# Performance work log

Measured on AMD Instinct MI355X. Metric: run time of the kernel, lower is better.

## Reference

```python
import jax, jax.numpy as jnp
import numpy as np

NUM_HEADS = 16
D_MODEL = 1024
D_K = D_MODEL // NUM_HEADS
EPS = 1e-6


def setup_inputs() -> dict:
    key = jax.random.key(0)
    ks = jax.random.split(key, 12)
    B, S, D = 8, 1024, D_MODEL
    scale = 0.02
    return {
        "query": jax.random.normal(ks[0], (B, S, D), dtype=jnp.float32),
        "key": jax.random.normal(ks[1], (B, S, D), dtype=jnp.float32),
        "value": jax.random.normal(ks[2], (B, S, D), dtype=jnp.float32),
        "policy": jax.random.uniform(ks[3], (B, S, 1), dtype=jnp.float32),
        "wq_w": jax.random.normal(ks[4], (D, D), dtype=jnp.float32) * scale,
        "wq_b": jnp.zeros((D,), dtype=jnp.float32),
        "wk_w": jax.random.normal(ks[5], (D, D), dtype=jnp.float32) * scale,
        "wk_b": jnp.zeros((D,), dtype=jnp.float32),
        "wv_w": jax.random.normal(ks[6], (D, D), dtype=jnp.float32) * scale,
        "wv_b": jnp.zeros((D,), dtype=jnp.float32),
        "dense_w": jax.random.normal(ks[7], (D, D), dtype=jnp.float32) * scale,
        "dense_b": jnp.zeros((D,), dtype=jnp.float32),
    }


def _split_heads(x):
    B, S, D = x.shape
    return x.reshape(B, S, NUM_HEADS, D_K).transpose(0, 2, 1, 3)  # [B,H,S,dk]


def reference(query, key, value, policy, wq_w, wq_b, wk_w, wk_b, wv_w, wv_b, dense_w, dense_b):
    B, S, D = query.shape
    # torch Linear: y = x @ W.T + b
    q = _split_heads(query @ wq_w.T + wq_b)
    k = _split_heads(key @ wk_w.T + wk_b)
    v = _split_heads(value @ wv_w.T + wv_b)

    scores = jnp.einsum("bhqd,bhkd->bhqk", q, k) / jnp.sqrt(jnp.float32(D_K))
    # policy branch: exp * policy normalization (no softmax max-subtraction, faithful)
    attn_policy = policy.reshape(B, 1, 1, S)
    sc = jnp.exp(scores) * attn_policy
    p_attn = (sc + EPS / S) / (jnp.sum(sc, axis=-1, keepdims=True) + EPS)

    x = jnp.einsum("bhqk,bhkd->bhqd", p_attn, v)
    x = x.transpose(0, 2, 1, 3).reshape(B, S, D)
    out = x @ dense_w.T + dense_b  # dropout = identity (eval mode)
    return out
```

## Files before the change

kernel.cpp:

```cpp
#include <hip/hip_runtime.h>


#define Sdim 1024
#define Ddim 1024

typedef unsigned short u16;
typedef float f32x4 __attribute__((ext_vector_type(4)));
typedef float f32x16 __attribute__((ext_vector_type(16)));
typedef __bf16 bf16x8 __attribute__((ext_vector_type(8)));
typedef u16 u16x8 __attribute__((ext_vector_type(8)));
typedef __attribute__((address_space(3))) void lds_void;
typedef __attribute__((address_space(1))) void gbl_void;

__device__ __forceinline__ u16 f2bf(float f) {
    unsigned u = __float_as_uint(f);
    u += 0x7fffu + ((u >> 16) & 1u);
    return (u16)(u >> 16);
}
__device__ __forceinline__ void gld16(const void* g, void* l) {
    __builtin_amdgcn_global_load_lds((const gbl_void*)g, (lds_void*)l, 16, 0, 0);
}
__device__ __forceinline__ unsigned pk_bf16(float lo, float hi) {
    const unsigned ul = __float_as_uint(lo) + 0x8000u;
    const unsigned uh = __float_as_uint(hi) + 0x8000u;
    return __builtin_amdgcn_perm(uh, ul, 0x07060302u);
}
#define MFMA16(a, b, c) __builtin_amdgcn_mfma_f32_16x16x32_bf16((a), (b), (c), 0, 0, 0)
#define MFMA32(a, b, c) __builtin_amdgcn_mfma_f32_32x32x16_bf16((a), (b), (c), 0, 0, 0)

__global__ __launch_bounds__(256) void cvt_all(const float* __restrict__ s0,
                                               const float* __restrict__ s1,
                                               const float* __restrict__ s2,
                                               const float* __restrict__ s3,
                                               const float* __restrict__ s4,
                                               const float* __restrict__ s5,
                                               const float* __restrict__ s6,
                                               u16* __restrict__ d0, u16* __restrict__ d1,
                                               u16* __restrict__ d2, u16* __restrict__ d3,
                                               u16* __restrict__ d4, u16* __restrict__ d5,
                                               u16* __restrict__ d6) {
    const int z = blockIdx.y;
    if (z >= 3 && blockIdx.x >= 512) return;
    const float* s = z == 0 ? s0 : z == 1 ? s1 : z == 2 ? s2 : z == 3 ? s3
                   : z == 4 ? s4 : z == 5 ? s5 : s6;
    u16* d = z == 0 ? d0 : z == 1 ? d1 : z == 2 ? d2 : z == 3 ? d3
           : z == 4 ? d4 : z == 5 ? d5 : d6;
    const float sc = (z == 3) ? 0.125f : 1.0f;
    const int i = (blockIdx.x * 256 + threadIdx.x) * 8;
    const float4 a = *(const float4*)(s + i);
    const float4 b = *(const float4*)(s + i + 4);
    u16x8 o;
    o[0] = f2bf(a.x * sc); o[1] = f2bf(a.y * sc); o[2] = f2bf(a.z * sc); o[3] = f2bf(a.w * sc);
    o[4] = f2bf(b.x * sc); o[5] = f2bf(b.y * sc); o[6] = f2bf(b.z * sc); o[7] = f2bf(b.w * sc);
    *(u16x8*)(d + i) = o;
}

template <int MODE>
__device__ __forceinline__ void gemm_core(const u16* __restrict__ A,
                                          const u16* __restrict__ W,
                                          const float* __restrict__ bias, float bscale,
                                          void* __restrict__ Cout,
                                          u16* sbuf, int m0, int n0) {
    u16* As = sbuf;
    u16* Bs = sbuf + 4096;
    const int tid  = threadIdx.x;
    const int wave = tid >> 6;
    const int lane = tid & 63;
    const int l15  = lane & 15;
    const int quad = lane >> 4;
    const int wm = (wave >> 1) * 64;
    const int wn = (wave & 1) * 64;

    const int e0 = wave * 512 + lane * 8;
    const int r0 = e0 >> 5, c0 = e0 & 31;
    const int e1 = 2048 + e0;
    const int r1 = e1 >> 5, c1 = e1 & 31;
    const u16* Ag0 = A + (size_t)(m0 + r0) * Ddim + c0;
    const u16* Ag1 = A + (size_t)(m0 + r1) * Ddim + c1;
    const u16* Wg0 = W + (size_t)(n0 + r0) * Ddim + c0;
    const u16* Wg1 = W + (size_t)(n0 + r1) * Ddim + c1;
    u16* As0 = As + wave * 512;
    u16* As1 = As + 2048 + wave * 512;
    u16* Bs0 = Bs + wave * 512;
    u16* Bs1 = Bs + 2048 + wave * 512;

    f32x4 acc[4][4] = {};

    for (int k0 = 0; k0 < Ddim; k0 += 32) {
        __syncthreads();
        gld16(Ag0 + k0, As0);
        gld16(Ag1 + k0, As1);
        gld16(Wg0 + k0, Bs0);
        gld16(Wg1 + k0, Bs1);
        __syncthreads();
        bf16x8 af[4], bfr[4];
#pragma unroll
        for (int i = 0; i < 4; ++i)
            af[i] = *(const bf16x8*)(As + (wm + i * 16 + l15) * 32 + quad * 8);
#pragma unroll
        for (int j = 0; j < 4; ++j)
            bfr[j] = *(const bf16x8*)(Bs + (wn + j * 16 + l15) * 32 + quad * 8);
#pragma unroll
        for (int i = 0; i < 4; ++i)
#pragma unroll
            for (int j = 0; j < 4; ++j)
                acc[i][j] = MFMA16(af[i], bfr[j], acc[i][j]);
    }

    float bv[4];
#pragma unroll
    for (int j = 0; j < 4; ++j) bv[j] = bias[n0 + wn + j * 16 + l15] * bscale;

    if (MODE == 2) {
        __syncthreads();
        u16* Ts = sbuf;
#pragma unroll
        for (int i = 0; i < 4; ++i)
#pragma unroll
            for (int j = 0; j < 4; ++j)
#pragma unroll
                for (int r = 0; r < 4; ++r)
                    Ts[(wm + i * 16 + quad * 4 + r) * 136 + wn + j * 16 + l15] =
                        f2bf(acc[i][j][r] + bv[j]);
        __syncthreads();
        const int orow = tid >> 1;
        const int p    = orow >> 6;
        const int dkl  = orow & 63;
        const int sh   = (tid & 1) * 64;
        const int bidx = m0 >> 10;
        const int s0   = m0 & 1023;
        const int h    = (n0 >> 6) + p;
        u16* dst = (u16*)Cout + ((size_t)((bidx * 16 + h) * 64 + dkl)) * Sdim + s0 + sh;
#pragma unroll
        for (int g = 0; g < 8; ++g) {
            u16x8 o;
#pragma unroll
            for (int j8 = 0; j8 < 8; ++j8)
                o[j8] = Ts[(sh + g * 8 + j8) * 136 + p * 64 + dkl];
            *(u16x8*)(dst + g * 8) = o;
        }
    } else {
#pragma unroll
        for (int i = 0; i < 4; ++i)
#pragma unroll
            for (int j = 0; j < 4; ++j)
#pragma unroll
                for (int r = 0; r < 4; ++r) {
                    const int row = m0 + wm + i * 16 + quad * 4 + r;
                    const int col = n0 + wn + j * 16 + l15;
                    const float v = acc[i][j][r] + bv[j];
                    if (MODE == 0)
                        ((u16*)Cout)[(size_t)row * Ddim + col] = f2bf(v);
                    else
                        ((float*)Cout)[(size_t)row * Ddim + col] = v;
                }
    }
}

__global__ __launch_bounds__(256) void gemm_qkv(const u16* __restrict__ A0, const u16* __restrict__ A1,
                                                const u16* __restrict__ A2,
                                                const u16* __restrict__ W0, const u16* __restrict__ W1,
                                                const u16* __restrict__ W2,
                                                const float* __restrict__ b0, const float* __restrict__ b1,
                                                const float* __restrict__ b2,
                                                u16* __restrict__ Qp, u16* __restrict__ Kp,
                                                u16* __restrict__ Vt) {
    __shared__ __align__(16) u16 sbuf[17408];
    const int z = blockIdx.z;
    const int m0 = blockIdx.x * 128, n0 = blockIdx.y * 128;
    if (z == 2) {
        gemm_core<2>(A2, W2, b2, 1.0f, (void*)Vt, sbuf, m0, n0);
    } else {
        const u16* A = z ? A1 : A0;
        const u16* W = z ? W1 : W0;
        const float* bias = z ? b1 : b0;
        u16* C = z ? Kp : Qp;
        gemm_core<0>(A, W, bias, z ? 1.0f : 0.125f, (void*)C, sbuf, m0, n0);
    }
}

__global__ __launch_bounds__(256) void gemm_dense(const u16* __restrict__ A,
                                                  const u16* __restrict__ W,
                                                  const float* __restrict__ bias,
                                                  float* __restrict__ C) {
    __shared__ __align__(16) u16 sbuf[8192];
    gemm_core<1>(A, W, bias, 1.0f, (void*)C, sbuf, blockIdx.x * 128, blockIdx.y * 128);
}

__global__ __launch_bounds__(256, 2) void attn_mfma(const u16* __restrict__ Qp,
                                                    const u16* __restrict__ Kp,
                                                    const u16* __restrict__ Vt,
                                                    const float* __restrict__ pol,
                                                    u16* __restrict__ Xb) {
    __shared__ __align__(16) u16 lds[28288];
    u16* Qs = lds;
    u16* Ks = lds + 18432;
    u16* Vs = lds + 23040;
    float* pols = (float*)(lds + 27648);
    float* denb = pols + 64;

    const int tid  = threadIdx.x;
    const int w    = tid >> 6;
    const int lane = tid & 63;
    const int l31  = lane & 31;
    const unsigned hsel = lane >> 5;
    const int q0 = blockIdx.x * 256;
    const int bh = blockIdx.y;
    const size_t bS = (size_t)(bh >> 4) * Sdim;
    const int col0 = (bh & 15) * 64;
    const int sr = tid >> 2;
    const int sc4 = tid & 3;

#pragma unroll
    for (int rg = 0; rg < 4; ++rg) {
        const int r = rg * 64 + sr;
#pragma unroll
        for (int g = 0; g < 2; ++g) {
            const int ch = sc4 + g * 4;
            *(u16x8*)(Qs + r * 72 + ch * 8) =
                *(const u16x8*)(Qp + (bS + q0 + r) * Ddim + col0 + ch * 8);
        }
    }
    __syncthreads();
    bf16x8 Qf[2][4];
#pragma unroll
    for (int qt = 0; qt < 2; ++qt)
#pragma unroll
        for (int dkt = 0; dkt < 4; ++dkt)
            Qf[qt][dkt] = *(const bf16x8*)(Qs + (w * 64 + qt * 32 + l31) * 72 +
                                           dkt * 16 + hsel * 8);

    f32x16 X[2][2] = {};
    float den[2] = {0.f, 0.f};

    for (int kt = 0; kt < 16; ++kt) {
        const int kbase = kt * 64;
        __syncthreads();
#pragma unroll
        for (int g = 0; g < 2; ++g) {
            const int ch = sc4 + g * 4;
            *(u16x8*)(Ks + sr * 72 + ch * 8) =
                *(const u16x8*)(Kp + (bS + kbase + sr) * Ddim + col0 + ch * 8);
            *(u16x8*)(Vs + sr * 72 + ch * 8) =
                *(const u16x8*)(Vt + ((size_t)(bh * 64 + sr)) * Sdim + kbase + ch * 8);
        }
        if (tid < 64) pols[tid] = pol[bS + kbase + tid];
        __syncthreads();

#pragma unroll
        for (int t32 = 0; t32 < 2; ++t32) {
            float polv[16];
#pragma unroll
            for (int e = 0; e < 16; ++e)
                polv[e] = pols[t32 * 32 + (e & 3) + 8 * (e >> 2) + 4 * hsel];
            bf16x8 Kf[4];
#pragma unroll
            for (int dkt = 0; dkt < 4; ++dkt)
                Kf[dkt] = *(const bf16x8*)(Ks + (t32 * 32 + l31) * 72 +
                                           dkt * 16 + hsel * 8);
#pragma unroll
            for (int qt = 0; qt < 2; ++qt) {
                f32x16 S = {};
#pragma unroll
                for (int dkt = 0; dkt < 4; ++dkt)
                    S = MFMA32(Kf[dkt], Qf[qt][dkt], S);
                float p[16];
#pragma unroll
                for (int e = 0; e < 16; ++e) {
                    p[e] = __expf(S[e]) * polv[e];
                    den[qt] += p[e];
                }
                unsigned pk_[8], sw[8];
#pragma unroll
                for (int g = 0; g < 4; ++g) {
                    pk_[2 * g]     = pk_bf16(p[4 * g + 0], p[4 * g + 1]);
                    pk_[2 * g + 1] = pk_bf16(p[4 * g + 2], p[4 * g + 3]);
                }
#pragma unroll
                for (int i = 0; i < 8; ++i)
                    sw[i] = (unsigned)__shfl_xor((int)pk_[i], 32);
#pragma unroll
                for (int tau = 0; tau < 2; ++tau) {
                    union { unsigned u[4]; bf16x8 v; } Af;
                    Af.u[0] = hsel ? sw[(2 * tau + 1) * 2 + 0] : pk_[(2 * tau) * 2 + 0];
                    Af.u[1] = hsel ? sw[(2 * tau + 1) * 2 + 1] : pk_[(2 * tau) * 2 + 1];
                    Af.u[2] = hsel ? pk_[(2 * tau + 1) * 2 + 0] : sw[(2 * tau) * 2 + 0];
                    Af.u[3] = hsel ? pk_[(2 * tau + 1) * 2 + 1] : sw[(2 * tau) * 2 + 1];
#pragma unroll
                    for (int ndt = 0; ndt < 2; ++ndt) {
                        const bf16x8 Vf =
                            *(const bf16x8*)(Vs + (ndt * 32 + l31) * 72 +
                                             t32 * 32 + tau * 16 + hsel * 8);
                        X[qt][ndt] = MFMA32(Af.v, Vf, X[qt][ndt]);
                    }
                }
            }
        }
    }

#pragma unroll
    for (int qt = 0; qt < 2; ++qt) {
        den[qt] += __shfl_xor(den[qt], 32);
        denb[w * 64 + qt * 32 + l31] = 1.0f / (den[qt] + 1e-6f);
    }
    u16* Xout = Qs;
#pragma unroll
    for (int qt = 0; qt < 2; ++qt) {
        float invv[16];
#pragma unroll
        for (int e = 0; e < 16; ++e)
            invv[e] = denb[w * 64 + qt * 32 + (e & 3) + 8 * (e >> 2) + 4 * hsel];
#pragma unroll
        for (int ndt = 0; ndt < 2; ++ndt)
#pragma unroll
            for (int e = 0; e < 16; ++e) {
                const int rho = (e & 3) + 8 * (e >> 2) + 4 * hsel;
                Xout[(w * 64 + qt * 32 + rho) * 72 + ndt * 32 + l31] =
                    f2bf(X[qt][ndt][e] * invv[e]);
            }
    }
    __syncthreads();
#pragma unroll
    for (int rg = 0; rg < 4; ++rg) {
        const int r = rg * 64 + sr;
#pragma unroll
        for (int g = 0; g < 2; ++g) {
            const int ch = sc4 + g * 4;
            *(u16x8*)(Xb + (bS + q0 + r) * Ddim + col0 + ch * 8) =
                *(const u16x8*)(Xout + r * 72 + ch * 8);
        }
    }
}

extern "C" void kernel_launch(void* const* d_in, const int* in_sizes, int n_in,
                              void* d_out, int out_size, void* d_ws, size_t ws_size,
                              hipStream_t stream) {
    const float* query   = (const float*)d_in[0];
    const float* key     = (const float*)d_in[1];
    const float* value   = (const float*)d_in[2];
    const float* policy  = (const float*)d_in[3];
    const float* wq_w    = (const float*)d_in[4];
    const float* wq_b    = (const float*)d_in[5];
    const float* wk_w    = (const float*)d_in[6];
    const float* wk_b    = (const float*)d_in[7];
    const float* wv_w    = (const float*)d_in[8];
    const float* wv_b    = (const float*)d_in[9];
    const float* dense_w = (const float*)d_in[10];
    const float* dense_b = (const float*)d_in[11];

    const size_t MM = 1u << 20;
    const size_t A8 = 8 * MM;
    u16* qa  = (u16*)d_ws;
    u16* ka  = qa + A8;
    u16* va  = ka + A8;
    u16* wqb = va + A8;
    u16* wkb = wqb + MM;
    u16* wvb = wkb + MM;
    u16* wdb = wvb + MM;
    u16* Qp  = wdb + MM;
    u16* Kp  = Qp + A8;
    u16* Vtg = Kp + A8;
    u16* Xb  = qa;

    cvt_all<<<dim3(4096, 7), 256, 0, stream>>>(query, key, value, wq_w, wk_w, wv_w, dense_w,
                                               qa, ka, va, wqb, wkb, wvb, wdb);

    gemm_qkv<<<dim3(64, 8, 3), 256, 0, stream>>>(qa, ka, va, wqb, wkb, wvb,
                                                 wq_b, wk_b, wv_b, Qp, Kp, Vtg);

    attn_mfma<<<dim3(4, 128), 256, 0, stream>>>(Qp, Kp, Vtg, policy, Xb);

    gemm_dense<<<dim3(64, 8), 256, 0, stream>>>(Xb, wdb, dense_b, (float*)d_out);
}
```

Measured before the change: 309.9 us.

## Shrink LDS footprint in QKV GEMM and attention, use exp2 with folded scale

The V-transpose epilogue in the QKV GEMM now stages the tile in two halves, so the shared buffer halves in size. The attention kernel no longer stages Q through LDS; it loads Q fragments straight from global memory and writes the output through a half-size buffer in two passes, cutting LDS from about 56KB to about 20KB to allow more resident blocks. log2(e) is folded into the Q scale so the softmax uses the native exp2. Policy and inverse-denominator reads are vectorized, and V fragments are hoisted out of the qt loop. The cost is extra barriers and uncoalesced direct Q loads.

```diff
diff --git a/kernel.cpp b/kernel.cpp
--- a/kernel.cpp
+++ b/kernel.cpp
@@ -3,6 +3,7 @@
 
 #define Sdim 1024
 #define Ddim 1024
+#define QSCALE 0.18033688f
 
 typedef unsigned short u16;
 typedef float f32x4 __attribute__((ext_vector_type(4)));
@@ -45,7 +46,7 @@
                    : z == 4 ? s4 : z == 5 ? s5 : s6;
     u16* d = z == 0 ? d0 : z == 1 ? d1 : z == 2 ? d2 : z == 3 ? d3
            : z == 4 ? d4 : z == 5 ? d5 : d6;
-    const float sc = (z == 3) ? 0.125f : 1.0f;
+    const float sc = (z == 3) ? QSCALE : 1.0f;
     const int i = (blockIdx.x * 256 + threadIdx.x) * 8;
     const float4 a = *(const float4*)(s + i);
     const float4 b = *(const float4*)(s + i + 4);
@@ -112,32 +113,37 @@
     for (int j = 0; j < 4; ++j) bv[j] = bias[n0 + wn + j * 16 + l15] * bscale;
 
     if (MODE == 2) {
-        __syncthreads();
         u16* Ts = sbuf;
-#pragma unroll
-        for (int i = 0; i < 4; ++i)
-#pragma unroll
-            for (int j = 0; j < 4; ++j)
-#pragma unroll
-                for (int r = 0; r < 4; ++r)
-                    Ts[(wm + i * 16 + quad * 4 + r) * 136 + wn + j * 16 + l15] =
-                        f2bf(acc[i][j][r] + bv[j]);
-        __syncthreads();
         const int orow = tid >> 1;
-        const int p    = orow >> 6;
-        const int dkl  = orow & 63;
-        const int sh   = (tid & 1) * 64;
+        const int sh2  = (tid & 1) * 32;
         const int bidx = m0 >> 10;
         const int s0   = m0 & 1023;
-        const int h    = (n0 >> 6) + p;
-        u16* dst = (u16*)Cout + ((size_t)((bidx * 16 + h) * 64 + dkl)) * Sdim + s0 + sh;
-#pragma unroll
-        for (int g = 0; g < 8; ++g) {
-            u16x8 o;
-#pragma unroll
-            for (int j8 = 0; j8 < 8; ++j8)
-                o[j8] = Ts[(sh + g * 8 + j8) * 136 + p * 64 + dkl];
-            *(u16x8*)(dst + g * 8) = o;
+        const int h    = (n0 >> 6) + (orow >> 6);
+        const int dkl  = orow & 63;
+#pragma unroll
+        for (int p = 0; p < 2; ++p) {
+            __syncthreads();
+            if ((wave >> 1) == p) {
+#pragma unroll
+                for (int i = 0; i < 4; ++i)
+#pragma unroll
+                    for (int j = 0; j < 4; ++j)
+#pragma unroll
+                        for (int r = 0; r < 4; ++r)
+                            Ts[(i * 16 + quad * 4 + r) * 136 + wn + j * 16 + l15] =
+                                f2bf(acc[i][j][r] + bv[j]);
+            }
+            __syncthreads();
+            u16* dst = (u16*)Cout +
+                ((size_t)((bidx * 16 + h) * 64 + dkl)) * Sdim + s0 + p * 64 + sh2;
+#pragma unroll
+            for (int g = 0; g < 4; ++g) {
+                u16x8 o;
+#pragma unroll
+                for (int j8 = 0; j8 < 8; ++j8)
+                    o[j8] = Ts[(sh2 + g * 8 + j8) * 136 + orow];
+                *(u16x8*)(dst + g * 8) = o;
+            }
         }
     } else {
 #pragma unroll
@@ -165,7 +171,7 @@
                                                 const float* __restrict__ b2,
                                                 u16* __restrict__ Qp, u16* __restrict__ Kp,
                                                 u16* __restrict__ Vt) {
-    __shared__ __align__(16) u16 sbuf[17408];
+    __shared__ __align__(16) u16 sbuf[8704];
     const int z = blockIdx.z;
     const int m0 = blockIdx.x * 128, n0 = blockIdx.y * 128;
     if (z == 2) {
@@ -175,7 +181,7 @@
         const u16* W = z ? W1 : W0;
         const float* bias = z ? b1 : b0;
         u16* C = z ? Kp : Qp;
-        gemm_core<0>(A, W, bias, z ? 1.0f : 0.125f, (void*)C, sbuf, m0, n0);
+        gemm_core<0>(A, W, bias, z ? 1.0f : QSCALE, (void*)C, sbuf, m0, n0);
     }
 }
 
@@ -192,18 +198,18 @@
                                                     const u16* __restrict__ Vt,
                                                     const float* __restrict__ pol,
                                                     u16* __restrict__ Xb) {
-    __shared__ __align__(16) u16 lds[28288];
-    u16* Qs = lds;
-    u16* Ks = lds + 18432;
-    u16* Vs = lds + 23040;
-    float* pols = (float*)(lds + 27648);
+    __shared__ __align__(16) u16 lds[9856];
+    u16* Ks = lds;
+    u16* Vs = lds + 4608;
+    u16* outb = lds;
+    float* pols = (float*)(lds + 9216);
     float* denb = pols + 64;
 
     const int tid  = threadIdx.x;
     const int w    = tid >> 6;
     const int lane = tid & 63;
     const int l31  = lane & 31;
-    const unsigned hsel = lane >> 5;
+    const int hsel = lane >> 5;
     const int q0 = blockIdx.x * 256;
     const int bh = blockIdx.y;
     const size_t bS = (size_t)(bh >> 4) * Sdim;
@@ -211,24 +217,13 @@
     const int sr = tid >> 2;
     const int sc4 = tid & 3;
 
-#pragma unroll
-    for (int rg = 0; rg < 4; ++rg) {
-        const int r = rg * 64 + sr;
-#pragma unroll
-        for (int g = 0; g < 2; ++g) {
-            const int ch = sc4 + g * 4;
-            *(u16x8*)(Qs + r * 72 + ch * 8) =
-                *(const u16x8*)(Qp + (bS + q0 + r) * Ddim + col0 + ch * 8);
-        }
-    }
-    __syncthreads();
     bf16x8 Qf[2][4];
 #pragma unroll
     for (int qt = 0; qt < 2; ++qt)
 #pragma unroll
         for (int dkt = 0; dkt < 4; ++dkt)
-            Qf[qt][dkt] = *(const bf16x8*)(Qs + (w * 64 + qt * 32 + l31) * 72 +
-                                           dkt * 16 + hsel * 8);
+            Qf[qt][dkt] = *(const bf16x8*)(Qp + (bS + q0 + w * 64 + qt * 32 + l31) * Ddim +
+                                           col0 + dkt * 16 + hsel * 8);
 
     f32x16 X[2][2] = {};
     float den[2] = {0.f, 0.f};
@@ -249,15 +244,21 @@
 
 #pragma unroll
         for (int t32 = 0; t32 < 2; ++t32) {
-            float polv[16];
-#pragma unroll
-            for (int e = 0; e < 16; ++e)
-                polv[e] = pols[t32 * 32 + (e & 3) + 8 * (e >> 2) + 4 * hsel];
+            f32x4 pv4[4];
+#pragma unroll
+            for (int j = 0; j < 4; ++j)
+                pv4[j] = *(const f32x4*)&pols[t32 * 32 + 8 * j + 4 * hsel];
             bf16x8 Kf[4];
 #pragma unroll
             for (int dkt = 0; dkt < 4; ++dkt)
-                Kf[dkt] = *(const bf16x8*)(Ks + (t32 * 32 + l31) * 72 +
-                                           dkt * 16 + hsel * 8);
+                Kf[dkt] = *(const bf16x8*)(Ks + (t32 * 32 + l31) * 72 + dkt * 16 + hsel * 8);
+            bf16x8 Vf[2][2];
+#pragma unroll
+            for (int tau = 0; tau < 2; ++tau)
+#pragma unroll
+                for (int ndt = 0; ndt < 2; ++ndt)
+                    Vf[tau][ndt] = *(const bf16x8*)(Vs + (ndt * 32 + l31) * 72 +
+                                                    t32 * 32 + tau * 16 + hsel * 8);
 #pragma unroll
             for (int qt = 0; qt < 2; ++qt) {
                 f32x16 S = {};
@@ -267,7 +268,7 @@
                 float p[16];
 #pragma unroll
                 for (int e = 0; e < 16; ++e) {
-                    p[e] = __expf(S[e]) * polv[e];
+                    p[e] = __builtin_amdgcn_exp2f(S[e]) * pv4[e >> 2][e & 3];
                     den[qt] += p[e];
                 }
                 unsigned pk_[8], sw[8];
@@ -287,48 +288,52 @@
                     Af.u[2] = hsel ? pk_[(2 * tau + 1) * 2 + 0] : sw[(2 * tau) * 2 + 0];
                     Af.u[3] = hsel ? pk_[(2 * tau + 1) * 2 + 1] : sw[(2 * tau) * 2 + 1];
 #pragma unroll
-                    for (int ndt = 0; ndt < 2; ++ndt) {
-                        const bf16x8 Vf =
-                            *(const bf16x8*)(Vs + (ndt * 32 + l31) * 72 +
-                                             t32 * 32 + tau * 16 + hsel * 8);
-                        X[qt][ndt] = MFMA32(Af.v, Vf, X[qt][ndt]);
-                    }
+                    for (int ndt = 0; ndt < 2; ++ndt)
+                        X[qt][ndt] = MFMA32(Af.v, Vf[tau][ndt], X[qt][ndt]);
                 }
             }
         }
     }
 
+    __syncthreads();
 #pragma unroll
     for (int qt = 0; qt < 2; ++qt) {
         den[qt] += __shfl_xor(den[qt], 32);
-        denb[w * 64 + qt * 32 + l31] = 1.0f / (den[qt] + 1e-6f);
-    }
-    u16* Xout = Qs;
+        if (lane < 32) denb[w * 64 + qt * 32 + l31] = 1.0f / (den[qt] + 1e-6f);
+    }
+    float invv[2][16];
 #pragma unroll
     for (int qt = 0; qt < 2; ++qt) {
-        float invv[16];
-#pragma unroll
-        for (int e = 0; e < 16; ++e)
-            invv[e] = denb[w * 64 + qt * 32 + (e & 3) + 8 * (e >> 2) + 4 * hsel];
-#pragma unroll
-        for (int ndt = 0; ndt < 2; ++ndt)
-#pragma unroll
-            for (int e = 0; e < 16; ++e) {
-                const int rho = (e & 3) + 8 * (e >> 2) + 4 * hsel;
-                Xout[(w * 64 + qt * 32 + rho) * 72 + ndt * 32 + l31] =
-                    f2bf(X[qt][ndt][e] * invv[e]);
-            }
-    }
-    __syncthreads();
-#pragma unroll
-    for (int rg = 0; rg < 4; ++rg) {
-        const int r = rg * 64 + sr;
-#pragma unroll
-        for (int g = 0; g < 2; ++g) {
-            const int ch = sc4 + g * 4;
-            *(u16x8*)(Xb + (bS + q0 + r) * Ddim + col0 + ch * 8) =
-                *(const u16x8*)(Xout + r * 72 + ch * 8);
-        }
+        f32x4 iv4[4];
+#pragma unroll
+        for (int j = 0; j < 4; ++j)
+            iv4[j] = *(const f32x4*)&denb[w * 64 + qt * 32 + 8 * j + 4 * hsel];
+#pragma unroll
+        for (int e = 0; e < 16; ++e) invv[qt][e] = iv4[e >> 2][e & 3];
+    }
+    const int cr = tid >> 1;
+    const int chalf = (tid & 1) * 32;
+#pragma unroll
+    for (int p = 0; p < 2; ++p) {
+        if ((w >> 1) == p) {
+#pragma unroll
+            for (int qt = 0; qt < 2; ++qt)
+#pragma unroll
+                for (int ndt = 0; ndt < 2; ++ndt)
+#pragma unroll
+                    for (int e = 0; e < 16; ++e) {
+                        const int rho = (e & 3) + 8 * (e >> 2) + 4 * hsel;
+                        outb[((w & 1) * 64 + qt * 32 + rho) * 72 + ndt * 32 + l31] =
+                            f2bf(X[qt][ndt][e] * invv[qt][e]);
+                    }
+        }
+        __syncthreads();
+#pragma unroll
+        for (int g = 0; g < 4; ++g) {
+            const u16x8 o = *(const u16x8*)(outb + cr * 72 + chalf + g * 8);
+            *(u16x8*)(Xb + (bS + q0 + p * 128 + cr) * Ddim + col0 + chalf + g * 8) = o;
+        }
+        __syncthreads();
     }
 }
 
```

Measured after the change: 322.4 us. 4.0% more time.
